# Kernel optimization log

Hardware: AMD Instinct MI355X
Metric: run time of the kernel (lower is better)

The kernel has to match this reference:

```python
import jax, jax.numpy as jnp
import numpy as np

N = 100_000        # nodes
E = 1_600_000      # edges (avg degree 16)
FN, FE = 32, 16    # node / edge feature dims
H = 64             # hidden_dim
C = 2              # num_classes
BN_EPS = 1e-5


def _lin(key, fan_in, fan_out):
    k1, k2 = jax.random.split(key)
    lim = 1.0 / np.sqrt(fan_in)
    w = jax.random.uniform(k1, (fan_in, fan_out), jnp.float32, -lim, lim)
    b = jax.random.uniform(k2, (fan_out,), jnp.float32, -lim, lim)
    return w, b


def setup_inputs() -> dict:
    key = jax.random.key(0)
    ks = jax.random.split(key, 20)
    inp = {}
    inp["x"] = jax.random.normal(ks[0], (N, FN), jnp.float32)
    inp["edge_attr"] = jax.random.normal(ks[1], (E, FE), jnp.float32)
    dims = [FN + FE, H, H]
    ki = 2
    for l in range(3):
        w1, b1 = _lin(ks[ki], dims[l], H); ki += 1
        w2, b2 = _lin(ks[ki], H, H); ki += 1
        inp[f"w1_{l}"], inp[f"b1_{l}"] = w1, b1
        inp[f"w2_{l}"], inp[f"b2_{l}"] = w2, b2
        inp[f"g_{l}"] = jnp.ones((H,), jnp.float32)   # BN gamma
        inp[f"be_{l}"] = jnp.zeros((H,), jnp.float32)  # BN beta
    cw1, cb1 = _lin(ks[ki], H, H // 2); ki += 1
    cw2, cb2 = _lin(ks[ki], H // 2, C); ki += 1
    inp["cw1"], inp["cb1"], inp["cw2"], inp["cb2"] = cw1, cb1, cw2, cb2
    inp["edge_index"] = jax.random.randint(ks[ki], (2, E), 0, N, jnp.int32)
    inp["batch"] = jnp.zeros((N,), jnp.int32)
    return inp


def _forward(x, edge_attr,
             w1_0, b1_0, w2_0, b2_0, g_0, be_0,
             w1_1, b1_1, w2_1, b2_1, g_1, be_1,
             w1_2, b1_2, w2_2, b2_2, g_2, be_2,
             cw1, cb1, cw2, cb2, edge_index):
    n = x.shape[0]
    row, col = edge_index[0], edge_index[1]
    seg = jax.ops.segment_sum

    # edge scatter-mean onto source node (row)
    edge_agg = seg(edge_attr, row, num_segments=n)              # [N, FE]
    counts = seg(jnp.ones((row.shape[0], 1), x.dtype), row, num_segments=n)
    edge_agg = edge_agg / jnp.maximum(counts, 1.0)
    h = jnp.concatenate([x, edge_agg], axis=1)                  # [N, FN+FE]

    layers = [(w1_0, b1_0, w2_0, b2_0, g_0, be_0),
              (w1_1, b1_1, w2_1, b2_1, g_1, be_1),
              (w1_2, b1_2, w2_2, b2_2, g_2, be_2)]
    for w1, b1, w2, b2, g, be in layers:
        # GINConv (eps=0): mlp(x_i + sum_{j->i} x_j), messages flow source->target
        agg = seg(h[row], col, num_segments=n)                  # gather + scatter-sum
        z = h + agg
        z = jax.nn.relu(z @ w1 + b1) @ w2 + b2                  # GIN MLP
        mu = jnp.mean(z, axis=0)                                # BatchNorm1d (batch stats)
        var = jnp.var(z, axis=0)
        z = (z - mu) * jax.lax.rsqrt(var + BN_EPS) * g + be
        h = jax.nn.relu(z)                                      # dropout = identity (eval)

    # global_mean_pool with all-zero batch ids -> single-graph mean
    pooled = jnp.mean(h, axis=0, keepdims=True)                 # [1, H]
    out = jax.nn.relu(pooled @ cw1 + cb1) @ cw2 + cb2           # [1, C]
    return out


def reference(x, edge_attr,
              w1_0, b1_0, w2_0, b2_0, g_0, be_0,
              w1_1, b1_1, w2_1, b2_1, g_1, be_1,
              w1_2, b1_2, w2_2, b2_2, g_2, be_2,
              cw1, cb1, cw2, cb2, edge_index, batch):
    return _forward(x, edge_attr,
                    w1_0, b1_0, w2_0, b2_0, g_0, be_0,
                    w1_1, b1_1, w2_1, b2_1, g_1, be_1,
                    w1_2, b1_2, w2_2, b2_2, g_2, be_2,
                    cw1, cb1, cw2, cb2, edge_index)
```

## Files before the change

kernel.cpp:

```cpp
#include <hip/hip_runtime.h>
#include <hip/hip_bf16.h>

#define NN 100000
#define EE 1600000
#define GRID_MLP 768
#define SCAN_T 1024

__device__ __forceinline__ float bf2f(unsigned short b) {
    return __uint_as_float(((unsigned int)b) << 16);
}
__device__ __forceinline__ void atomAddF(float* p, float v) {
    unsafeAtomicAdd(p, v);
}
__device__ __forceinline__ int clampN(int i) {
    return min(max(i, 0), NN - 1);
}

__global__ void k_probe(const unsigned int* __restrict__ g0,
                        const unsigned int* __restrict__ ea,
                        int* __restrict__ flags) {
    int lane = threadIdx.x & 63;
    unsigned int w = ea[(long)lane * 199999];
    unsigned int e = (w >> 8) & 0x7F;
    bool sane = (e >= 0x30 && e <= 0x47);
    unsigned long long m = __ballot(sane);
    if (lane == 0) {
        int bfW = (g0[0] != 0x3F800000u) ? 1 : 0;
        int bfX = (__popcll(m) >= 32) ? 1 : 0;
        flags[0] = bfW;
        flags[1] = bfX;
        flags[2] = (bfW | bfX);
    }
}

__global__ __launch_bounds__(256) void k_edge_mean(const void* __restrict__ ea,
                                                   const int* __restrict__ row,
                                                   float* __restrict__ edge_agg,
                                                   float* __restrict__ counts,
                                                   const int* __restrict__ flags) {
    const int bfX = flags[1];
    int sub = (threadIdx.x & 63) >> 4;
    int f   = threadIdx.x & 15;
    long gw = (long)((blockIdx.x * blockDim.x + threadIdx.x) >> 6);
    long nw = (long)((gridDim.x * blockDim.x) >> 6);
    const unsigned short* eau = (const unsigned short*)ea;
    const float* eaf = (const float*)ea;
    for (long e0 = gw * 4; e0 < EE; e0 += nw * 4) {
        long e = e0 + sub;
        if (e < EE) {
            int r = clampN(row[e]);
            float v = bfX ? bf2f(eau[e * 16 + f]) : eaf[e * 16 + f];
            atomAddF(&edge_agg[(long)r * 16 + f], v);
            if (f == 0) atomAddF(&counts[r], 1.0f);
        }
    }
}

__global__ __launch_bounds__(256) void k_build_h0(const void* __restrict__ x,
                                                  const float* __restrict__ edge_agg,
                                                  const float* __restrict__ counts,
                                                  float* __restrict__ h,
                                                  const int* __restrict__ flags) {
    const int bfX = flags[1];
    long total = (long)NN * 16;
    long stride = (long)gridDim.x * blockDim.x;
    for (long t = blockIdx.x * blockDim.x + threadIdx.x; t < total; t += stride) {
        long node = t >> 4;
        int c = (int)(t & 15);
        float4 v = make_float4(0.f, 0.f, 0.f, 0.f);
        if (c < 8) {
            if (bfX) {
                uint2 u = *(const uint2*)((const unsigned short*)x + node * 32 + c * 4);
                v.x = __uint_as_float(u.x << 16);
                v.y = __uint_as_float(u.x & 0xffff0000u);
                v.z = __uint_as_float(u.y << 16);
                v.w = __uint_as_float(u.y & 0xffff0000u);
            } else {
                v = *(const float4*)((const float*)x + node * 32 + c * 4);
            }
        } else if (c < 12) {
            float r = 1.0f / fmaxf(counts[node], 1.0f);
            float4 a = *(const float4*)&edge_agg[node * 16 + (c - 8) * 4];
            v.x = a.x * r; v.y = a.y * r; v.z = a.z * r; v.w = a.w * r;
        }
        *(float4*)&h[node * 64 + c * 4] = v;
    }
}

__global__ __launch_bounds__(256) void k_hist(const int* __restrict__ col,
                                              int* __restrict__ deg) {
    long t = (long)blockIdx.x * 256 + threadIdx.x;
    long stride = (long)gridDim.x * 256;
    for (long e = t; e < EE; e += stride) atomicAdd(&deg[clampN(col[e])], 1);
}

__global__ __launch_bounds__(SCAN_T) void k_scan(const int* __restrict__ deg,
                                                 int* __restrict__ rowstart,
                                                 int* __restrict__ cursor) {
    __shared__ int part[SCAN_T];
    int t = threadIdx.x;
    const int chunk = (NN + SCAN_T - 1) / SCAN_T;
    int lo = t * chunk, hi = min(lo + chunk, NN);
    int s = 0;
    for (int i = lo; i < hi; ++i) s += deg[i];
    part[t] = s;
    __syncthreads();
    for (int off = 1; off < SCAN_T; off <<= 1) {
        int v = part[t];
        if (t >= off) v += part[t - off];
        __syncthreads();
        part[t] = v;
        __syncthreads();
    }
    int run = (t > 0) ? part[t - 1] : 0;
    for (int i = lo; i < hi; ++i) {
        rowstart[i] = run;
        cursor[i] = run;
        run += deg[i];
    }
}

__global__ __launch_bounds__(256) void k_scatter(const int* __restrict__ row,
                                                 const int* __restrict__ col,
                                                 int* __restrict__ cursor,
                                                 int* __restrict__ esrc) {
    long t = (long)blockIdx.x * 256 + threadIdx.x;
    long stride = (long)gridDim.x * 256;
    for (long e = t; e < EE; e += stride) {
        int c = clampN(col[e]);
        int pos = atomicAdd(&cursor[c], 1);
        esrc[pos] = clampN(row[e]);
    }
}

template <int BNIN>
__global__ __launch_bounds__(256) void k_agg(const float* __restrict__ zin,
                                             const float* __restrict__ bnv,
                                             const int* __restrict__ rowstart,
                                             const int* __restrict__ deg,
                                             const int* __restrict__ esrc,
                                             float* __restrict__ agg) {
    int lane = threadIdx.x & 63;
    int c = (int)(((long)blockIdx.x * 256 + threadIdx.x) >> 6);
    if (c >= NN) return;
    float sc = BNIN ? bnv[lane] : 0.f;
    float sh = BNIN ? bnv[64 + lane] : 0.f;
    int s0 = rowstart[c];
    int d = deg[c];
    float acc = 0.f;
    int j = 0;
    for (; j + 1 < d; j += 2) {
        int r0 = esrc[s0 + j];
        int r1 = esrc[s0 + j + 1];
        float v0 = zin[(long)r0 * 64 + lane];
        float v1 = zin[(long)r1 * 64 + lane];
        if (BNIN) {
            v0 = fmaxf(fmaf(v0, sc, sh), 0.f);
            v1 = fmaxf(fmaf(v1, sc, sh), 0.f);
        }
        acc += v0 + v1;
    }
    if (j < d) {
        int r = esrc[s0 + j];
        float v = zin[(long)r * 64 + lane];
        if (BNIN) v = fmaxf(fmaf(v, sc, sh), 0.f);
        acc += v;
    }
    agg[(long)c * 64 + lane] = acc;
}

template <int KD, int BNIN>
__global__ __launch_bounds__(256) void k_mlp(const float* __restrict__ xin,
                                             float* az,
                                             const void* __restrict__ w1,
                                             const void* __restrict__ b1,
                                             const void* __restrict__ w2,
                                             const void* __restrict__ b2,
                                             float* __restrict__ stats,
                                             const float* __restrict__ bnv,
                                             const int* __restrict__ flags) {
    __shared__ float w1s[KD * 64];
    __shared__ float w2s[64 * 64];
    __shared__ float b1s[64], b2s[64];
    __shared__ float inb[4][4][68];
    __shared__ float t1b[4][4][68];
    const int bfW = flags[0];
    const unsigned short* w1u = (const unsigned short*)w1;
    const unsigned short* w2u = (const unsigned short*)w2;
    const float* w1f = (const float*)w1;
    const float* w2f = (const float*)w2;
    for (int i = threadIdx.x; i < KD * 64; i += 256) w1s[i] = bfW ? bf2f(w1u[i]) : w1f[i];
    for (int i = threadIdx.x; i < 64 * 64; i += 256) w2s[i] = bfW ? bf2f(w2u[i]) : w2f[i];
    if (threadIdx.x < 64) {
        b1s[threadIdx.x] = bfW ? bf2f(((const unsigned short*)b1)[threadIdx.x])
                               : ((const float*)b1)[threadIdx.x];
        b2s[threadIdx.x] = bfW ? bf2f(((const unsigned short*)b2)[threadIdx.x])
                               : ((const float*)b2)[threadIdx.x];
    }
    __syncthreads();

    int wv = threadIdx.x >> 6, lane = threadIdx.x & 63;
    int q = lane >> 4;
    int cg = lane & 15;
    int ks = cg * 4;
    float4 sc4 = make_float4(0.f, 0.f, 0.f, 0.f), sh4 = sc4;
    if (BNIN) {
        sc4 = *(const float4*)&bnv[ks];
        sh4 = *(const float4*)&bnv[64 + ks];
    }
    long gw = (long)blockIdx.x * 4 + wv;
    long nw = (long)gridDim.x * 4;
    float s[4] = {0.f, 0.f, 0.f, 0.f}, sq[4] = {0.f, 0.f, 0.f, 0.f};

    for (long base = gw * 4; base < NN; base += nw * 4) {
        long r = base + q;
        float4 hv = make_float4(0.f, 0.f, 0.f, 0.f);
        if (r < NN) {
            float4 a = *(const float4*)&xin[r * 64 + ks];
            if (BNIN) {
                a.x = fmaxf(fmaf(a.x, sc4.x, sh4.x), 0.f);
                a.y = fmaxf(fmaf(a.y, sc4.y, sh4.y), 0.f);
                a.z = fmaxf(fmaf(a.z, sc4.z, sh4.z), 0.f);
                a.w = fmaxf(fmaf(a.w, sc4.w, sh4.w), 0.f);
            }
            float4 b = *(const float4*)&az[r * 64 + ks];
            hv = make_float4(a.x + b.x, a.y + b.y, a.z + b.z, a.w + b.w);
        }
        *(float4*)&inb[wv][q][ks] = hv;

        float4 acc = make_float4(b1s[ks], b1s[ks + 1], b1s[ks + 2], b1s[ks + 3]);
        for (int k = 0; k < KD; ++k) {
            float ik = inb[wv][q][k];
            float4 w = *(const float4*)&w1s[k * 64 + ks];
            acc.x = fmaf(ik, w.x, acc.x); acc.y = fmaf(ik, w.y, acc.y);
            acc.z = fmaf(ik, w.z, acc.z); acc.w = fmaf(ik, w.w, acc.w);
        }
        acc.x = fmaxf(acc.x, 0.f); acc.y = fmaxf(acc.y, 0.f);
        acc.z = fmaxf(acc.z, 0.f); acc.w = fmaxf(acc.w, 0.f);
        *(float4*)&t1b[wv][q][ks] = acc;

        float4 a2 = make_float4(b2s[ks], b2s[ks + 1], b2s[ks + 2], b2s[ks + 3]);
        for (int k = 0; k < 64; ++k) {
            float tk = t1b[wv][q][k];
            float4 w = *(const float4*)&w2s[k * 64 + ks];
            a2.x = fmaf(tk, w.x, a2.x); a2.y = fmaf(tk, w.y, a2.y);
            a2.z = fmaf(tk, w.z, a2.z); a2.w = fmaf(tk, w.w, a2.w);
        }
        if (r < NN) {
            *(float4*)&az[r * 64 + ks] = a2;
            s[0] += a2.x; s[1] += a2.y; s[2] += a2.z; s[3] += a2.w;
            sq[0] += a2.x * a2.x; sq[1] += a2.y * a2.y;
            sq[2] += a2.z * a2.z; sq[3] += a2.w * a2.w;
        }
    }
    #pragma unroll
    for (int j = 0; j < 4; ++j) {
        for (int m = 16; m < 64; m <<= 1) {
            s[j] += __shfl_xor(s[j], m);
            sq[j] += __shfl_xor(sq[j], m);
        }
    }
    __syncthreads();
    float* red = &t1b[0][0][0];
    if (lane < 16) {
        #pragma unroll
        for (int j = 0; j < 4; ++j) {
            red[wv * 128 + cg * 4 + j] = s[j];
            red[wv * 128 + 64 + cg * 4 + j] = sq[j];
        }
    }
    __syncthreads();
    for (int i = threadIdx.x; i < 128; i += 256) {
        atomAddF(&stats[i], red[i] + red[128 + i] + red[256 + i] + red[384 + i]);
    }
}

__global__ void k_bnstats(const float* __restrict__ stats,
                          const void* __restrict__ g,
                          const void* __restrict__ be,
                          float* __restrict__ bn,
                          const int* __restrict__ flags) {
    const int bfW = flags[0];
    int f = threadIdx.x;
    if (f >= 64) return;
    float s = stats[f];
    float sq = stats[64 + f];
    const float invN = 1.0f / NN;
    float mu = s * invN;
    float var = sq * invN - mu * mu;
    float inv = rsqrtf(var + 1e-5f);
    float gv = bfW ? bf2f(((const unsigned short*)g)[f]) : ((const float*)g)[f];
    float bv = bfW ? bf2f(((const unsigned short*)be)[f]) : ((const float*)be)[f];
    float sc = inv * gv;
    bn[f] = sc;
    bn[64 + f] = bv - mu * sc;
}

__global__ __launch_bounds__(256) void k_pool(const float* __restrict__ z,
                                              const float* __restrict__ bnv,
                                              float* __restrict__ pooled) {
    long t0 = (long)blockIdx.x * blockDim.x + threadIdx.x;
    long stride = (long)gridDim.x * blockDim.x;
    int c = (int)(t0 & 15);
    float4 sc = *(const float4*)&bnv[c * 4];
    float4 sh = *(const float4*)&bnv[64 + c * 4];
    float4 ps = make_float4(0.f, 0.f, 0.f, 0.f);
    for (long t = t0; t < (long)NN * 16; t += stride) {
        float4 zv = *(const float4*)&z[(t >> 4) * 64 + c * 4];
        ps.x += fmaxf(fmaf(zv.x, sc.x, sh.x), 0.f);
        ps.y += fmaxf(fmaf(zv.y, sc.y, sh.y), 0.f);
        ps.z += fmaxf(fmaf(zv.z, sc.z, sh.z), 0.f);
        ps.w += fmaxf(fmaf(zv.w, sc.w, sh.w), 0.f);
    }
    for (int m = 16; m < 64; m <<= 1) {
        ps.x += __shfl_xor(ps.x, m); ps.y += __shfl_xor(ps.y, m);
        ps.z += __shfl_xor(ps.z, m); ps.w += __shfl_xor(ps.w, m);
    }
    if ((threadIdx.x & 63) < 16) {
        atomAddF(&pooled[c * 4 + 0], ps.x);
        atomAddF(&pooled[c * 4 + 1], ps.y);
        atomAddF(&pooled[c * 4 + 2], ps.z);
        atomAddF(&pooled[c * 4 + 3], ps.w);
    }
}

__global__ void k_head(const float* __restrict__ pooled,
                       const void* __restrict__ cw1,
                       const void* __restrict__ cb1,
                       const void* __restrict__ cw2,
                       const void* __restrict__ cb2,
                       void* __restrict__ out,
                       const int* __restrict__ flags) {
    const int bfW = flags[0];
    const int outBf = flags[2];
    int lane = threadIdx.x & 63;
    const unsigned short* cw1u = (const unsigned short*)cw1;
    const unsigned short* cw2u = (const unsigned short*)cw2;
    const float* cw1f = (const float*)cw1;
    const float* cw2f = (const float*)cw2;
    const float invN = 1.0f / NN;
    float t1 = 0.f;
    if (lane < 32) {
        float acc = bfW ? bf2f(((const unsigned short*)cb1)[lane]) : ((const float*)cb1)[lane];
        for (int f = 0; f < 64; ++f) {
            float w = bfW ? bf2f(cw1u[f * 32 + lane]) : cw1f[f * 32 + lane];
            acc = fmaf(pooled[f] * invN, w, acc);
        }
        t1 = fmaxf(acc, 0.f);
    }
    float w0 = 0.f, w1v = 0.f;
    if (lane < 32) {
        w0  = bfW ? bf2f(cw2u[lane * 2 + 0]) : cw2f[lane * 2 + 0];
        w1v = bfW ? bf2f(cw2u[lane * 2 + 1]) : cw2f[lane * 2 + 1];
    }
    float p0 = t1 * w0;
    float p1 = t1 * w1v;
    for (int m = 1; m < 64; m <<= 1) {
        p0 += __shfl_xor(p0, m);
        p1 += __shfl_xor(p1, m);
    }
    if (lane == 0) {
        float c0 = bfW ? bf2f(((const unsigned short*)cb2)[0]) : ((const float*)cb2)[0];
        float c1 = bfW ? bf2f(((const unsigned short*)cb2)[1]) : ((const float*)cb2)[1];
        if (outBf) {
            ((__hip_bfloat16*)out)[0] = __float2bfloat16(p0 + c0);
            ((__hip_bfloat16*)out)[1] = __float2bfloat16(p1 + c1);
        } else {
            ((float*)out)[0] = p0 + c0;
            ((float*)out)[1] = p1 + c1;
        }
    }
}

extern "C" void kernel_launch(void* const* d_in, const int* in_sizes, int n_in,
                              void* d_out, int out_size, void* d_ws, size_t ws_size,
                              hipStream_t stream) {
    const void* x  = d_in[0];
    const void* ea = d_in[1];
    const void* w1[3] = {d_in[2], d_in[8], d_in[14]};
    const void* b1[3] = {d_in[3], d_in[9], d_in[15]};
    const void* w2[3] = {d_in[4], d_in[10], d_in[16]};
    const void* b2[3] = {d_in[5], d_in[11], d_in[17]};
    const void* g[3]  = {d_in[6], d_in[12], d_in[18]};
    const void* be[3] = {d_in[7], d_in[13], d_in[19]};
    const void* cw1 = d_in[20];
    const void* cb1 = d_in[21];
    const void* cw2 = d_in[22];
    const void* cb2 = d_in[23];
    const int* ei = (const int*)d_in[24];
    const int* row = ei;
    const int* col = ei + EE;

    float* ws = (float*)d_ws;
    float* edge_agg = ws;
    float* counts   = ws + 1600000;
    float* pooled   = ws + 1700000;
    float* bn       = ws + 1700064;
    float* stats    = ws + 1700448;
    int*   flags    = (int*)(ws + 1700832);
    int*   rowstart = (int*)(ws + 1700848);
    int*   cursor   = (int*)(ws + 1800848);
    float* H        = ws + 1900848;
    float* A        = H + (long)NN * 64;
    int*   esrc     = (int*)edge_agg;
    int*   deg      = (int*)counts;

    hipMemsetAsync(ws, 0, (size_t)1700848 * sizeof(float), stream);
    k_probe<<<1, 64, 0, stream>>>((const unsigned int*)g[0], (const unsigned int*)ea, flags);

    k_edge_mean<<<1024, 256, 0, stream>>>(ea, row, edge_agg, counts, flags);
    k_build_h0<<<1024, 256, 0, stream>>>(x, edge_agg, counts, H, flags);

    hipMemsetAsync(deg, 0, (size_t)NN * sizeof(int), stream);
    k_hist<<<2048, 256, 0, stream>>>(col, deg);
    k_scan<<<1, SCAN_T, 0, stream>>>(deg, rowstart, cursor);
    k_scatter<<<2048, 256, 0, stream>>>(row, col, cursor, esrc);

    k_agg<0><<<25000, 256, 0, stream>>>(H, nullptr, rowstart, deg, esrc, A);
    k_mlp<48, 0><<<GRID_MLP, 256, 0, stream>>>(H, A, w1[0], b1[0], w2[0], b2[0],
                                               stats + 0, nullptr, flags);
    k_bnstats<<<1, 64, 0, stream>>>(stats + 0, g[0], be[0], bn + 0, flags);

    k_agg<1><<<25000, 256, 0, stream>>>(A, bn + 0, rowstart, deg, esrc, H);
    k_mlp<64, 1><<<GRID_MLP, 256, 0, stream>>>(A, H, w1[1], b1[1], w2[1], b2[1],
                                               stats + 128, bn + 0, flags);
    k_bnstats<<<1, 64, 0, stream>>>(stats + 128, g[1], be[1], bn + 128, flags);

    k_agg<1><<<25000, 256, 0, stream>>>(H, bn + 128, rowstart, deg, esrc, A);
    k_mlp<64, 1><<<GRID_MLP, 256, 0, stream>>>(H, A, w1[2], b1[2], w2[2], b2[2],
                                               stats + 256, bn + 128, flags);
    k_bnstats<<<1, 64, 0, stream>>>(stats + 256, g[2], be[2], bn + 256, flags);

    k_pool<<<512, 256, 0, stream>>>(A, bn + 256, pooled);
    k_head<<<1, 64, 0, stream>>>(pooled, cw1, cb1, cw2, cb2, d_out, flags);
}
```

Measured before the change: 1.383 ms.

## Replace single-block degree scan with three-pass multi-block scan

The exclusive prefix sum over node degrees ran in one 1024-thread block, each thread walking a sequential chunk of about 98 entries twice with strided, uncoalesced accesses. It now runs as three passes: per-block reductions, a single-block scan of the 391 partial sums, and a per-block local scan that writes rowstart and cursor. This spreads the work across many CUs with coalesced loads, at the cost of two extra kernel launches and a small workspace buffer that shifts the H offset.

```diff
diff --git a/kernel.cpp b/kernel.cpp
--- a/kernel.cpp
+++ b/kernel.cpp
@@ -4,7 +4,8 @@
 #define NN 100000
 #define EE 1600000
 #define GRID_MLP 768
-#define SCAN_T 1024
+#define SCHUNK 256
+#define SBLOCKS ((NN + SCHUNK - 1) / SCHUNK)
 
 __device__ __forceinline__ float bf2f(unsigned short b) {
     return __uint_as_float(((unsigned int)b) << 16);
@@ -94,29 +95,56 @@
     for (long e = t; e < EE; e += stride) atomicAdd(&deg[clampN(col[e])], 1);
 }
 
-__global__ __launch_bounds__(SCAN_T) void k_scan(const int* __restrict__ deg,
-                                                 int* __restrict__ rowstart,
-                                                 int* __restrict__ cursor) {
-    __shared__ int part[SCAN_T];
+__global__ __launch_bounds__(256) void k_scan1(const int* __restrict__ deg,
+                                               int* __restrict__ part) {
+    __shared__ int red[4];
+    int b = blockIdx.x;
+    int i = b * SCHUNK + threadIdx.x;
+    int v = (i < NN) ? deg[i] : 0;
+    for (int m = 1; m < 64; m <<= 1) v += __shfl_xor(v, m);
+    if ((threadIdx.x & 63) == 0) red[threadIdx.x >> 6] = v;
+    __syncthreads();
+    if (threadIdx.x == 0) part[b] = red[0] + red[1] + red[2] + red[3];
+}
+
+__global__ __launch_bounds__(512) void k_scan2(int* __restrict__ part) {
+    __shared__ int s[512];
     int t = threadIdx.x;
-    const int chunk = (NN + SCAN_T - 1) / SCAN_T;
-    int lo = t * chunk, hi = min(lo + chunk, NN);
-    int s = 0;
-    for (int i = lo; i < hi; ++i) s += deg[i];
-    part[t] = s;
-    __syncthreads();
-    for (int off = 1; off < SCAN_T; off <<= 1) {
-        int v = part[t];
-        if (t >= off) v += part[t - off];
+    int v = (t < SBLOCKS) ? part[t] : 0;
+    s[t] = v;
+    __syncthreads();
+    for (int off = 1; off < 512; off <<= 1) {
+        int u = s[t];
+        int w = (t >= off) ? s[t - off] : 0;
         __syncthreads();
-        part[t] = v;
+        s[t] = u + w;
         __syncthreads();
     }
-    int run = (t > 0) ? part[t - 1] : 0;
-    for (int i = lo; i < hi; ++i) {
-        rowstart[i] = run;
-        cursor[i] = run;
-        run += deg[i];
+    if (t < SBLOCKS) part[t] = s[t] - v;
+}
+
+__global__ __launch_bounds__(256) void k_scan3(const int* __restrict__ deg,
+                                               const int* __restrict__ part,
+                                               int* __restrict__ rowstart,
+                                               int* __restrict__ cursor) {
+    __shared__ int s[256];
+    int b = blockIdx.x;
+    int i = b * SCHUNK + threadIdx.x;
+    int t = threadIdx.x;
+    int v = (i < NN) ? deg[i] : 0;
+    s[t] = v;
+    __syncthreads();
+    for (int off = 1; off < 256; off <<= 1) {
+        int u = s[t];
+        int w = (t >= off) ? s[t - off] : 0;
+        __syncthreads();
+        s[t] = u + w;
+        __syncthreads();
+    }
+    if (i < NN) {
+        int r = part[b] + s[t] - v;
+        rowstart[i] = r;
+        cursor[i] = r;
     }
 }
 
@@ -400,7 +428,8 @@
     int*   flags    = (int*)(ws + 1700832);
     int*   rowstart = (int*)(ws + 1700848);
     int*   cursor   = (int*)(ws + 1800848);
-    float* H        = ws + 1900848;
+    int*   spart    = (int*)(ws + 1900848);
+    float* H        = ws + 1901360;
     float* A        = H + (long)NN * 64;
     int*   esrc     = (int*)edge_agg;
     int*   deg      = (int*)counts;
@@ -413,7 +442,9 @@
 
     hipMemsetAsync(deg, 0, (size_t)NN * sizeof(int), stream);
     k_hist<<<2048, 256, 0, stream>>>(col, deg);
-    k_scan<<<1, SCAN_T, 0, stream>>>(deg, rowstart, cursor);
+    k_scan1<<<SBLOCKS, 256, 0, stream>>>(deg, spart);
+    k_scan2<<<1, 512, 0, stream>>>(spart);
+    k_scan3<<<SBLOCKS, 256, 0, stream>>>(deg, spart, rowstart, cursor);
     k_scatter<<<2048, 256, 0, stream>>>(row, col, cursor, esrc);
 
     k_agg<0><<<25000, 256, 0, stream>>>(H, nullptr, rowstart, deg, esrc, A);
```

New measurement: 1.171 ms. -15.3%, faster.
